# Performance work log

Measured on AMD Instinct MI355X. Metric: run time of the kernel, lower is better.

## Reference

```python
import jax, jax.numpy as jnp
import numpy as np

N, E, F_IN, F_HID, F_OUT = 100000, 1600000, 128, 128, 64


def setup_inputs() -> dict:
    key = jax.random.key(0)
    k = jax.random.split(key, 6)
    x = jax.random.normal(k[0], (N, F_IN), dtype=jnp.float32)
    edge_index = jax.random.randint(k[1], (2, E), 0, N, dtype=jnp.int32)
    # Glorot-ish init for the two GCNConv linear layers (+ bias, PyG default bias=True)
    W1 = jax.random.normal(k[2], (F_IN, F_HID), dtype=jnp.float32) * (1.0 / np.sqrt(F_IN))
    b1 = jnp.zeros((F_HID,), dtype=jnp.float32)
    W2 = jax.random.normal(k[3], (F_HID, F_OUT), dtype=jnp.float32) * (1.0 / np.sqrt(F_HID))
    b2 = jnp.zeros((F_OUT,), dtype=jnp.float32)
    return {"x": x, "edge_index": edge_index, "W1": W1, "b1": b1, "W2": W2, "b2": b2}


def reference(x, edge_index, W1, b1, W2, b2):
    n = x.shape[0]
    row, col = edge_index[0], edge_index[1]
    # gcn_norm with add_self_loops=True, edge_weight=None -> all-ones weights
    loop = jnp.arange(n, dtype=row.dtype)
    row = jnp.concatenate([row, loop])
    col = jnp.concatenate([col, loop])
    w = jnp.ones(row.shape[0], dtype=x.dtype)
    deg = jax.ops.segment_sum(w, col, num_segments=n)  # in-degree at targets
    dis = jnp.where(deg > 0, jax.lax.rsqrt(jnp.maximum(deg, 1.0)), 0.0)
    norm = dis[row] * w * dis[col]  # [E+N]

    def gcn_conv(h, W, b):
        h = h @ W                       # linear transform first (PyG order)
        msg = h[row] * norm[:, None]    # gather + scale, [E+N, d]
        return jax.ops.segment_sum(msg, col, num_segments=n) + b  # scatter-add

    h = jax.nn.relu(gcn_conv(x, W1, b1))
    # dropout is identity in eval mode
    return gcn_conv(h, W2, b2)
```

## Files before the change

kernel.cpp:

```cpp
#include <hip/hip_runtime.h>

#define F1 128
#define F2 64
#define BSH 9
#define BSZ 512
#define BFILL_CAP 12288
#define PSTAGE 2048

typedef unsigned int u32;
typedef unsigned short u16;
typedef __attribute__((ext_vector_type(8))) short bf16x8;
typedef __attribute__((ext_vector_type(4))) float f32x4;

__device__ __forceinline__ u32 bf16rne(float f) {
    u32 u = __float_as_uint(f);
    return (u + 0x7FFFu + ((u >> 16) & 1u)) >> 16;
}
__device__ __forceinline__ u32 pack2(float lo, float hi) {
    return bf16rne(lo) | (bf16rne(hi) << 16);
}
__device__ __forceinline__ float bflo(u32 u) { return __uint_as_float(u << 16); }
__device__ __forceinline__ float bfhi(u32 u) { return __uint_as_float(u & 0xFFFF0000u); }

__device__ __forceinline__ void acc8(float* ax, uint4 v) {
    ax[0] += bflo(v.x); ax[1] += bfhi(v.x);
    ax[2] += bflo(v.y); ax[3] += bfhi(v.y);
    ax[4] += bflo(v.z); ax[5] += bfhi(v.z);
    ax[6] += bflo(v.w); ax[7] += bfhi(v.w);
}

__device__ __forceinline__ void facc8(float* ax, uint4 v, float w) {
    ax[0] = fmaf(w, bflo(v.x), ax[0]); ax[1] = fmaf(w, bfhi(v.x), ax[1]);
    ax[2] = fmaf(w, bflo(v.y), ax[2]); ax[3] = fmaf(w, bfhi(v.y), ax[3]);
    ax[4] = fmaf(w, bflo(v.z), ax[4]); ax[5] = fmaf(w, bfhi(v.z), ax[5]);
    ax[6] = fmaf(w, bflo(v.w), ax[6]); ax[7] = fmaf(w, bfhi(v.w), ax[7]);
}


__device__ __forceinline__ void wprep_do(const float* __restrict__ W,
                                         uint4* __restrict__ wf, int NBc, int t) {
    int lane = t & 63;
    int rem = t >> 6;
    int nb = rem % NBc;
    int kb = rem / NBc;
    int C = NBc * 16;
    int col = nb * 16 + (lane & 15);
    int krow = kb * 32 + (lane >> 4) * 8;
    u32 w[4];
#pragma unroll
    for (int p = 0; p < 4; p++) {
        float lo = W[(size_t)(krow + 2 * p) * C + col];
        float hi = W[(size_t)(krow + 2 * p + 1) * C + col];
        w[p] = pack2(lo, hi);
    }
    wf[t] = make_uint4(w[0], w[1], w[2], w[3]);
}


__global__ __launch_bounds__(256) void k_hw(const int* __restrict__ colv,
                                            int* __restrict__ bucket_cnt,
                                            const float* __restrict__ W1,
                                            const float* __restrict__ W2,
                                            uint4* __restrict__ w1f,
                                            uint4* __restrict__ w2f, int E) {
    __shared__ int l[256];
    int blk = blockIdx.x;
    int t = threadIdx.x;
    if (blk < 256) {
        l[t] = 0;
        __syncthreads();
        for (int e = blk * 256 + t; e < E; e += 256 * 256)
            atomicAdd(&l[colv[e] >> BSH], 1);
        __syncthreads();
        if (l[t]) atomicAdd(&bucket_cnt[t], l[t]);
    } else {
        int b2 = blk - 256;
        if (b2 < 8) wprep_do(W1, w1f, 8, b2 * 256 + t);
        else        wprep_do(W2, w2f, 4, (b2 - 8) * 256 + t);
    }
}


__global__ __launch_bounds__(256, 4) void k_pg(const int* __restrict__ rowv,
                                               const int* __restrict__ colv,
                                               const int* __restrict__ bucket_cnt,
                                               int* __restrict__ bucket_cur,
                                               u32* __restrict__ ebuf, int E, int PB,
                                               const float* __restrict__ x,
                                               const uint4* __restrict__ w1f,
                                               u16* __restrict__ gb, int N) {
    if ((int)blockIdx.x < PB) {
        __shared__ int lcnt[256], lexcl[256], lcur[256], lbase[256], gscan[256];
        __shared__ int stot;
        __shared__ u32 sval[PSTAGE];
        __shared__ u16 sbkt[PSTAGE];
        int t = threadIdx.x;
        lcnt[t] = 0;
        __syncthreads();
        int rows[8], cols[8];
        int e0 = blockIdx.x * PSTAGE;
#pragma unroll
        for (int it = 0; it < 8; it++) {
            int e = e0 + it * 256 + t;
            bool v = e < E;
            cols[it] = v ? colv[e] : -1;
            rows[it] = v ? rowv[e] : 0;
            if (v) atomicAdd(&lcnt[cols[it] >> BSH], 1);
        }
        int bc = bucket_cnt[t];
        __syncthreads();
        int v = lcnt[t];
        lexcl[t] = v;
        gscan[t] = bc;
        __syncthreads();
        for (int d = 1; d < 256; d <<= 1) {
            int u1 = (t >= d) ? lexcl[t - d] : 0;
            int u2 = (t >= d) ? gscan[t - d] : 0;
            __syncthreads();
            lexcl[t] += u1;
            gscan[t] += u2;
            __syncthreads();
        }
        int incl = lexcl[t];
        int gincl = gscan[t];
        __syncthreads();
        lexcl[t] = incl - v;
        lcur[t] = incl - v;
        if (v) lbase[t] = (gincl - bc) + atomicAdd(&bucket_cur[t], v);
        if (t == 255) stot = incl;
        __syncthreads();
#pragma unroll
        for (int it = 0; it < 8; it++) {
            if (cols[it] >= 0) {
                int b = cols[it] >> BSH;
                int pos = atomicAdd(&lcur[b], 1);
                sval[pos] = ((u32)(cols[it] & (BSZ - 1)) << 17) | (u32)rows[it];
                sbkt[pos] = (u16)b;
            }
        }
        __syncthreads();
        int total = stot;
        for (int i = t; i < total; i += 256) {
            int b = sbkt[i];
            ebuf[lbase[b] + (i - lexcl[b])] = sval[i];
        }
    } else {
        int bid = (int)blockIdx.x - PB;
        int lane = threadIdx.x & 63;
        int wave = threadIdx.x >> 6;
        int m = lane & 15, quad = lane >> 4;
        int row0 = bid * 64 + wave * 16;
        int arow = min(row0 + m, N - 1);
        const float* xr = x + (size_t)arow * F1 + quad * 8;
        bf16x8 a[4];
#pragma unroll
        for (int kb = 0; kb < 4; kb++) {
            float4 lo = *(const float4*)(xr + kb * 32);
            float4 hi = *(const float4*)(xr + kb * 32 + 4);
            a[kb][0] = (short)bf16rne(lo.x); a[kb][1] = (short)bf16rne(lo.y);
            a[kb][2] = (short)bf16rne(lo.z); a[kb][3] = (short)bf16rne(lo.w);
            a[kb][4] = (short)bf16rne(hi.x); a[kb][5] = (short)bf16rne(hi.y);
            a[kb][6] = (short)bf16rne(hi.z); a[kb][7] = (short)bf16rne(hi.w);
        }
        f32x4 acc[8];
#pragma unroll
        for (int nb = 0; nb < 8; nb++) acc[nb] = (f32x4)(0.0f);
#pragma unroll
        for (int nb = 0; nb < 8; nb++) {
#pragma unroll
            for (int kb = 0; kb < 4; kb++) {
                uint4 braw = w1f[(kb * 8 + nb) * 64 + lane];
                bf16x8 bf = *(bf16x8*)&braw;
                acc[nb] = __builtin_amdgcn_mfma_f32_16x16x32_bf16(a[kb], bf, acc[nb], 0, 0, 0);
            }
        }
        int rbase = row0 + quad * 4;
#pragma unroll
        for (int reg = 0; reg < 4; reg++) {
            int r = rbase + reg;
            if (r < N) {
                u16* gr = gb + (size_t)r * F1 + m;
#pragma unroll
                for (int nb = 0; nb < 8; nb++)
                    gr[nb * 16] = (u16)bf16rne(acc[nb][reg]);
            }
        }
    }
}


__global__ __launch_bounds__(1024) void k_bfill(const u32* __restrict__ ebuf,
                                                const int* __restrict__ bucket_cnt,
                                                int* __restrict__ rowptr,
                                                float* __restrict__ dis,
                                                int* __restrict__ adj, int N, int E) {
    __shared__ int cnt[BSZ], scn[BSZ], cur[BSZ];
    __shared__ int bb[256];
    __shared__ int sadj[BFILL_CAP];
    int t = threadIdx.x;
    int b = blockIdx.x;
    if (t < 256) bb[t] = bucket_cnt[t];
    if (t < BSZ) cnt[t] = 0;
    __syncthreads();
    for (int d = 1; d < 256; d <<= 1) {
        int u = (t >= d && t < 256) ? bb[t - d] : 0;
        __syncthreads();
        if (t < 256) bb[t] += u;
        __syncthreads();
    }
    int e1 = bb[b];
    int e0 = e1 - bucket_cnt[b];
    int len = e1 - e0;
    if (b == 0 && t == 0) rowptr[N] = E;
    for (int i = e0 + t; i < e1; i += 1024)
        atomicAdd(&cnt[ebuf[i] >> 17], 1);
    __syncthreads();
    if (t < BSZ) scn[t] = cnt[t];
    __syncthreads();
    for (int d = 1; d < BSZ; d <<= 1) {
        int u = (t >= d && t < BSZ) ? scn[t - d] : 0;
        __syncthreads();
        if (t < BSZ) scn[t] += u;
        __syncthreads();
    }
    if (t < BSZ) {
        int excl = scn[t] - cnt[t];
        cur[t] = excl;
        int node = (b << BSH) + t;
        if (node < N) {
            rowptr[node] = e0 + excl;
            dis[node] = rsqrtf((float)(cnt[t] + 1));
        }
    }
    __syncthreads();
    if (len <= BFILL_CAP) {
        for (int i = e0 + t; i < e1; i += 1024) {
            u32 p = ebuf[i];
            int c = p >> 17;
            int pos = atomicAdd(&cur[c], 1);
            sadj[pos] = (int)(p & 0x1FFFFu);
        }
        __syncthreads();
        for (int i = t; i < len; i += 1024)
            adj[e0 + i] = sadj[i];
    } else {
        for (int i = e0 + t; i < e1; i += 1024) {
            u32 p = ebuf[i];
            int c = p >> 17;
            int pos = atomicAdd(&cur[c], 1);
            adj[e0 + pos] = (int)(p & 0x1FFFFu);
        }
    }
}


__global__ __launch_bounds__(256) void k_agg1(const uint4* __restrict__ g1,
                                              const int* __restrict__ rowptr,
                                              const int* __restrict__ adj,
                                              const float* __restrict__ dis,
                                              const float* __restrict__ b,
                                              uint4* __restrict__ z, int N) {
    int node = __builtin_amdgcn_readfirstlane(blockIdx.x * 4 + (threadIdx.x >> 6));
    if (node >= N) return;
    int lane = threadIdx.x & 63;
    int grp = lane >> 4;
    int sub = lane & 15;
    float ax[8];
#pragma unroll
    for (int i = 0; i < 8; i++) ax[i] = 0.0f;
    int s = rowptr[node], e = rowptr[node + 1];
    float dnode = dis[node];
    if (grp == 0) facc8(ax, g1[(size_t)node * 16 + sub], dnode);
    const uint4 z4 = make_uint4(0u, 0u, 0u, 0u);
    int i0 = s + grp;
    bool p0 = i0 < e, p1 = i0 + 4 < e, p2 = i0 + 8 < e, p3 = i0 + 12 < e;
    int c0 = 0, c1 = 0, c2 = 0, c3 = 0;
    float d0 = 0.0f, d1 = 0.0f, d2 = 0.0f, d3 = 0.0f;
    if (p0) { c0 = adj[i0];      d0 = dis[c0]; }
    if (p1) { c1 = adj[i0 + 4];  d1 = dis[c1]; }
    if (p2) { c2 = adj[i0 + 8];  d2 = dis[c2]; }
    if (p3) { c3 = adj[i0 + 12]; d3 = dis[c3]; }
    for (int j = s; j < e; j += 16) {
        uint4 v0 = z4, v1 = z4, v2 = z4, v3 = z4;
        if (p0) v0 = g1[(size_t)c0 * 16 + sub];
        if (p1) v1 = g1[(size_t)c1 * 16 + sub];
        if (p2) v2 = g1[(size_t)c2 * 16 + sub];
        if (p3) v3 = g1[(size_t)c3 * 16 + sub];
        float w0 = d0, w1 = d1, w2 = d2, w3 = d3;
        int in0 = j + 16 + grp;
        p0 = in0 < e; p1 = in0 + 4 < e; p2 = in0 + 8 < e; p3 = in0 + 12 < e;
        d0 = 0.0f; d1 = 0.0f; d2 = 0.0f; d3 = 0.0f;
        if (p0) { c0 = adj[in0];      d0 = dis[c0]; }
        if (p1) { c1 = adj[in0 + 4];  d1 = dis[c1]; }
        if (p2) { c2 = adj[in0 + 8];  d2 = dis[c2]; }
        if (p3) { c3 = adj[in0 + 12]; d3 = dis[c3]; }
        facc8(ax, v0, w0);
        facc8(ax, v1, w1);
        facc8(ax, v2, w2);
        facc8(ax, v3, w3);
    }
#pragma unroll
    for (int i = 0; i < 8; i++) {
        ax[i] += __shfl_xor(ax[i], 16);
        ax[i] += __shfl_xor(ax[i], 32);
    }
    if (grp == 0) {
        float4 b0 = *(const float4*)(b + 8 * sub);
        float4 b1 = *(const float4*)(b + 8 * sub + 4);
        float o[8];
        o[0] = fmaxf(fmaf(dnode, ax[0], b0.x), 0.0f);
        o[1] = fmaxf(fmaf(dnode, ax[1], b0.y), 0.0f);
        o[2] = fmaxf(fmaf(dnode, ax[2], b0.z), 0.0f);
        o[3] = fmaxf(fmaf(dnode, ax[3], b0.w), 0.0f);
        o[4] = fmaxf(fmaf(dnode, ax[4], b1.x), 0.0f);
        o[5] = fmaxf(fmaf(dnode, ax[5], b1.y), 0.0f);
        o[6] = fmaxf(fmaf(dnode, ax[6], b1.z), 0.0f);
        o[7] = fmaxf(fmaf(dnode, ax[7], b1.w), 0.0f);
        uint4 ov;
        ov.x = pack2(o[0], o[1]); ov.y = pack2(o[2], o[3]);
        ov.z = pack2(o[4], o[5]); ov.w = pack2(o[6], o[7]);
        z[(size_t)node * 16 + sub] = ov;
    }
}


__global__ __launch_bounds__(256, 4) void k_gemm2(const u32* __restrict__ z,
                                                  const uint4* __restrict__ w2f,
                                                  const float* __restrict__ dis,
                                                  u16* __restrict__ gb, int N) {
    int lane = threadIdx.x & 63;
    int wave = threadIdx.x >> 6;
    int m = lane & 15, quad = lane >> 4;
    int row0 = blockIdx.x * 64 + wave * 16;
    int arow = min(row0 + m, N - 1);
    const u32* zr = z + (size_t)arow * 64 + quad * 4;
    bf16x8 a[4];
#pragma unroll
    for (int kb = 0; kb < 4; kb++) {
        uint4 za = *(const uint4*)(zr + kb * 16);
        a[kb] = *(bf16x8*)&za;
    }
    f32x4 acc[4];
#pragma unroll
    for (int nb = 0; nb < 4; nb++) acc[nb] = (f32x4)(0.0f);
#pragma unroll
    for (int nb = 0; nb < 4; nb++) {
#pragma unroll
        for (int kb = 0; kb < 4; kb++) {
            uint4 braw = w2f[(kb * 4 + nb) * 64 + lane];
            bf16x8 bf = *(bf16x8*)&braw;
            acc[nb] = __builtin_amdgcn_mfma_f32_16x16x32_bf16(a[kb], bf, acc[nb], 0, 0, 0);
        }
    }
    float dv[4];
    int rbase = row0 + quad * 4;
#pragma unroll
    for (int reg = 0; reg < 4; reg++) dv[reg] = dis[min(rbase + reg, N - 1)];
#pragma unroll
    for (int reg = 0; reg < 4; reg++) {
        int r = rbase + reg;
        if (r < N) {
            u16* gr = gb + (size_t)r * F2 + m;
#pragma unroll
            for (int nb = 0; nb < 4; nb++)
                gr[nb * 16] = (u16)bf16rne(acc[nb][reg] * dv[reg]);
        }
    }
}


__global__ __launch_bounds__(256) void k_agg2(const uint4* __restrict__ g,
                                              const int* __restrict__ rowptr,
                                              const int* __restrict__ adj,
                                              const float* __restrict__ dis,
                                              const float* __restrict__ b,
                                              float* __restrict__ out, int N) {
    int node = __builtin_amdgcn_readfirstlane(blockIdx.x * 4 + (threadIdx.x >> 6));
    if (node >= N) return;
    int lane = threadIdx.x & 63;
    int grp = lane >> 3;
    int sub = lane & 7;
    float ax[8];
#pragma unroll
    for (int i = 0; i < 8; i++) ax[i] = 0.0f;
    int s = rowptr[node], e = rowptr[node + 1];
    if (grp == 0) acc8(ax, g[(size_t)node * 8 + sub]);
    const uint4 z4 = make_uint4(0u, 0u, 0u, 0u);
    int i0 = s + grp;
    bool p0 = i0 < e, p1 = i0 + 8 < e;
    int c0 = 0, c1 = 0;
    if (p0) c0 = adj[i0];
    if (p1) c1 = adj[i0 + 8];
    for (int j = s; j < e; j += 16) {
        uint4 v0 = z4, v1 = z4;
        if (p0) v0 = g[(size_t)c0 * 8 + sub];
        if (p1) v1 = g[(size_t)c1 * 8 + sub];
        int in0 = j + 16 + grp;
        p0 = in0 < e; p1 = in0 + 8 < e;
        if (p0) c0 = adj[in0];
        if (p1) c1 = adj[in0 + 8];
        acc8(ax, v0);
        acc8(ax, v1);
    }
#pragma unroll
    for (int i = 0; i < 8; i++) {
        ax[i] += __shfl_xor(ax[i], 8);
        ax[i] += __shfl_xor(ax[i], 16);
        ax[i] += __shfl_xor(ax[i], 32);
    }
    if (grp == 0) {
        float d = dis[node];
        float4 b0 = *(const float4*)(b + 8 * sub);
        float4 b1 = *(const float4*)(b + 8 * sub + 4);
        float4 o0, o1;
        o0.x = fmaf(d, ax[0], b0.x); o0.y = fmaf(d, ax[1], b0.y);
        o0.z = fmaf(d, ax[2], b0.z); o0.w = fmaf(d, ax[3], b0.w);
        o1.x = fmaf(d, ax[4], b1.x); o1.y = fmaf(d, ax[5], b1.y);
        o1.z = fmaf(d, ax[6], b1.z); o1.w = fmaf(d, ax[7], b1.w);
        float4* op = (float4*)(out + (size_t)node * F2 + 8 * sub);
        op[0] = o0;
        op[1] = o1;
    }
}


extern "C" void kernel_launch(void* const* d_in, const int* in_sizes, int n_in,
                              void* d_out, int out_size, void* d_ws, size_t ws_size,
                              hipStream_t stream) {
    const float* x  = (const float*)d_in[0];
    const int*   ei = (const int*)d_in[1];
    const float* W1 = (const float*)d_in[2];
    const float* b1 = (const float*)d_in[3];
    const float* W2 = (const float*)d_in[4];
    const float* b2 = (const float*)d_in[5];
    float* out = (float*)d_out;

    const int N = in_sizes[0] / F1;
    const int E = in_sizes[1] / 2;
    const int NB = (N + BSZ - 1) >> BSH;
    const int* rowv = ei;
    const int* colv = ei + E;

    char* ws = (char*)d_ws;
    size_t off = 0;
    auto take = [&](size_t bytes) -> void* {
        void* p = ws + off;
        off += (bytes + 255) & ~(size_t)255;
        return p;
    };
    u16*   g1b     = (u16*)take((size_t)N * F1 * 2);
    u32*   zb      = (u32*)take((size_t)N * 64 * 4);
    u16*   g2b     = g1b;
    u32*   ebuf    = zb;
    float* dis     = (float*)take((size_t)N * 4);
    int*   rowptr  = (int*)take((size_t)(N + 1) * 4);
    int*   adj     = (int*)take((size_t)E * 4);
    uint4* w1f     = (uint4*)take(4 * 8 * 64 * 16);
    uint4* w2f     = (uint4*)take(4 * 4 * 64 * 16);
    int*   bucket_cnt  = (int*)take(512 * 4);
    int*   bucket_cur  = bucket_cnt + 256;

    hipMemsetAsync(bucket_cnt, 0, 512 * 4, stream);

    k_hw<<<268, 256, 0, stream>>>(colv, bucket_cnt, W1, W2, w1f, w2f, E);

    int PB = (E + PSTAGE - 1) / PSTAGE;
    int gblocks = (N + 63) / 64;
    k_pg<<<PB + gblocks, 256, 0, stream>>>(rowv, colv, bucket_cnt, bucket_cur, ebuf,
                                           E, PB, x, w1f, g1b, N);

    k_bfill<<<NB, 1024, 0, stream>>>(ebuf, bucket_cnt, rowptr, dis, adj, N, E);

    k_agg1<<<(N + 3) / 4, 256, 0, stream>>>((const uint4*)g1b, rowptr, adj, dis, b1,
                                            (uint4*)zb, N);
    k_gemm2<<<gblocks, 256, 0, stream>>>(zb, w2f, dis, g2b, N);
    k_agg2<<<(N + 3) / 4, 256, 0, stream>>>((const uint4*)g2b, rowptr, adj, dis, b2, out, N);
}
```

Before: 272.0 us.

## Double partition stage size, use nontemporal adj loads, unroll agg2 gather 4-wide

The partition kernel now handles 4096 edges per block instead of 2048, so fewer blocks do more work each. Adjacency index loads in both aggregation kernels become nontemporal loads, which aims to keep the streamed CSR indices from evicting the gathered feature rows in cache. The layer-2 aggregation now gathers four neighbours per group per iteration instead of two, giving more loads in flight. The costs are more registers and shared memory in the partition kernel, which may lower occupancy, and fewer blocks for small tails.

```diff
diff --git a/kernel.cpp b/kernel.cpp
--- a/kernel.cpp
+++ b/kernel.cpp
@@ -5,7 +5,7 @@
 #define BSH 9
 #define BSZ 512
 #define BFILL_CAP 12288
-#define PSTAGE 2048
+#define PSTAGE 4096
 
 typedef unsigned int u32;
 typedef unsigned short u16;
@@ -97,10 +97,10 @@
         int t = threadIdx.x;
         lcnt[t] = 0;
         __syncthreads();
-        int rows[8], cols[8];
+        int rows[16], cols[16];
         int e0 = blockIdx.x * PSTAGE;
 #pragma unroll
-        for (int it = 0; it < 8; it++) {
+        for (int it = 0; it < 16; it++) {
             int e = e0 + it * 256 + t;
             bool v = e < E;
             cols[it] = v ? colv[e] : -1;
@@ -130,7 +130,7 @@
         if (t == 255) stot = incl;
         __syncthreads();
 #pragma unroll
-        for (int it = 0; it < 8; it++) {
+        for (int it = 0; it < 16; it++) {
             if (cols[it] >= 0) {
                 int b = cols[it] >> BSH;
                 int pos = atomicAdd(&lcur[b], 1);
@@ -276,10 +276,10 @@
     bool p0 = i0 < e, p1 = i0 + 4 < e, p2 = i0 + 8 < e, p3 = i0 + 12 < e;
     int c0 = 0, c1 = 0, c2 = 0, c3 = 0;
     float d0 = 0.0f, d1 = 0.0f, d2 = 0.0f, d3 = 0.0f;
-    if (p0) { c0 = adj[i0];      d0 = dis[c0]; }
-    if (p1) { c1 = adj[i0 + 4];  d1 = dis[c1]; }
-    if (p2) { c2 = adj[i0 + 8];  d2 = dis[c2]; }
-    if (p3) { c3 = adj[i0 + 12]; d3 = dis[c3]; }
+    if (p0) { c0 = __builtin_nontemporal_load(adj + i0);      d0 = dis[c0]; }
+    if (p1) { c1 = __builtin_nontemporal_load(adj + i0 + 4);  d1 = dis[c1]; }
+    if (p2) { c2 = __builtin_nontemporal_load(adj + i0 + 8);  d2 = dis[c2]; }
+    if (p3) { c3 = __builtin_nontemporal_load(adj + i0 + 12); d3 = dis[c3]; }
     for (int j = s; j < e; j += 16) {
         uint4 v0 = z4, v1 = z4, v2 = z4, v3 = z4;
         if (p0) v0 = g1[(size_t)c0 * 16 + sub];
@@ -290,10 +290,10 @@
         int in0 = j + 16 + grp;
         p0 = in0 < e; p1 = in0 + 4 < e; p2 = in0 + 8 < e; p3 = in0 + 12 < e;
         d0 = 0.0f; d1 = 0.0f; d2 = 0.0f; d3 = 0.0f;
-        if (p0) { c0 = adj[in0];      d0 = dis[c0]; }
-        if (p1) { c1 = adj[in0 + 4];  d1 = dis[c1]; }
-        if (p2) { c2 = adj[in0 + 8];  d2 = dis[c2]; }
-        if (p3) { c3 = adj[in0 + 12]; d3 = dis[c3]; }
+        if (p0) { c0 = __builtin_nontemporal_load(adj + in0);      d0 = dis[c0]; }
+        if (p1) { c1 = __builtin_nontemporal_load(adj + in0 + 4);  d1 = dis[c1]; }
+        if (p2) { c2 = __builtin_nontemporal_load(adj + in0 + 8);  d2 = dis[c2]; }
+        if (p3) { c3 = __builtin_nontemporal_load(adj + in0 + 12); d3 = dis[c3]; }
         facc8(ax, v0, w0);
         facc8(ax, v1, w1);
         facc8(ax, v2, w2);
@@ -387,20 +387,28 @@
     if (grp == 0) acc8(ax, g[(size_t)node * 8 + sub]);
     const uint4 z4 = make_uint4(0u, 0u, 0u, 0u);
     int i0 = s + grp;
-    bool p0 = i0 < e, p1 = i0 + 8 < e;
-    int c0 = 0, c1 = 0;
-    if (p0) c0 = adj[i0];
-    if (p1) c1 = adj[i0 + 8];
-    for (int j = s; j < e; j += 16) {
-        uint4 v0 = z4, v1 = z4;
+    bool p0 = i0 < e, p1 = i0 + 8 < e, p2 = i0 + 16 < e, p3 = i0 + 24 < e;
+    int c0 = 0, c1 = 0, c2 = 0, c3 = 0;
+    if (p0) c0 = __builtin_nontemporal_load(adj + i0);
+    if (p1) c1 = __builtin_nontemporal_load(adj + i0 + 8);
+    if (p2) c2 = __builtin_nontemporal_load(adj + i0 + 16);
+    if (p3) c3 = __builtin_nontemporal_load(adj + i0 + 24);
+    for (int j = s; j < e; j += 32) {
+        uint4 v0 = z4, v1 = z4, v2 = z4, v3 = z4;
         if (p0) v0 = g[(size_t)c0 * 8 + sub];
         if (p1) v1 = g[(size_t)c1 * 8 + sub];
-        int in0 = j + 16 + grp;
-        p0 = in0 < e; p1 = in0 + 8 < e;
-        if (p0) c0 = adj[in0];
-        if (p1) c1 = adj[in0 + 8];
+        if (p2) v2 = g[(size_t)c2 * 8 + sub];
+        if (p3) v3 = g[(size_t)c3 * 8 + sub];
+        int in0 = j + 32 + grp;
+        p0 = in0 < e; p1 = in0 + 8 < e; p2 = in0 + 16 < e; p3 = in0 + 24 < e;
+        if (p0) c0 = __builtin_nontemporal_load(adj + in0);
+        if (p1) c1 = __builtin_nontemporal_load(adj + in0 + 8);
+        if (p2) c2 = __builtin_nontemporal_load(adj + in0 + 16);
+        if (p3) c3 = __builtin_nontemporal_load(adj + in0 + 24);
         acc8(ax, v0);
         acc8(ax, v1);
+        acc8(ax, v2);
+        acc8(ax, v3);
     }
 #pragma unroll
     for (int i = 0; i < 8; i++) {
```

Result: no change. 272.3 us (+0.1%).
